# Kernel optimization log

Measured on AMD Instinct MI355X. Metric: run time of the kernel, lower is better.

Reference implementation:

```python
import jax, jax.numpy as jnp
import numpy as np

FEAT_DIM = 4
TOKEN_DIM = 256
HIDDEN = [256, 256]
B, N, T = 512, 512, 4
BN_EPS = 1e-5


def setup_inputs() -> dict:
    key = jax.random.key(0)
    ks = jax.random.split(key, 10)
    bbox_ltwh = jax.random.uniform(ks[0], (B, N, T, FEAT_DIM), dtype=jnp.float32)
    mask = jax.random.randint(ks[1], (B, N), 0, 2).astype(bool)
    # MLP params: Linear(4->256)+BN+ReLU, Linear(256->256)+BN+ReLU, Linear(256->256)
    def lin(k, fan_in, fan_out):
        bound = 1.0 / np.sqrt(fan_in)
        kw, kb = jax.random.split(k)
        W = jax.random.uniform(kw, (fan_in, fan_out), minval=-bound, maxval=bound, dtype=jnp.float32)
        b = jax.random.uniform(kb, (fan_out,), minval=-bound, maxval=bound, dtype=jnp.float32)
        return W, b
    W1, b1 = lin(ks[2], FEAT_DIM, HIDDEN[0])
    W2, b2 = lin(ks[3], HIDDEN[0], HIDDEN[1])
    W3, b3 = lin(ks[4], HIDDEN[1], TOKEN_DIM)
    g1 = jnp.ones((HIDDEN[0],), jnp.float32); be1 = jnp.zeros((HIDDEN[0],), jnp.float32)
    g2 = jnp.ones((HIDDEN[1],), jnp.float32); be2 = jnp.zeros((HIDDEN[1],), jnp.float32)
    return {"bbox_ltwh": bbox_ltwh, "mask": mask,
            "W1": W1, "b1": b1, "g1": g1, "be1": be1,
            "W2": W2, "b2": b2, "g2": g2, "be2": be2,
            "W3": W3, "b3": b3}


def _masked_bn(h, m, cnt, gamma, beta):
    # BatchNorm1d (training mode) over only the valid (masked-in) rows.
    mu = jnp.sum(h * m, axis=0) / cnt
    var = jnp.sum(jnp.square(h - mu) * m, axis=0) / cnt
    return (h - mu) * jax.lax.rsqrt(var + BN_EPS) * gamma + beta


def reference(bbox_ltwh, mask, W1, b1, g1, be1, W2, b2, g2, be2, W3, b3):
    # last bbox of each tracklet: [B, N, 4] -> [B*N, 4]
    x = bbox_ltwh[:, :, 0].reshape(-1, FEAT_DIM)
    m = mask.reshape(-1).astype(x.dtype)[:, None]  # [B*N, 1]
    cnt = jnp.maximum(jnp.sum(m), 1.0)
    # Equivalent to gather(valid) -> MLP -> scatter into zeros: compute on all
    # rows with BN statistics taken over valid rows only, then zero invalid rows.
    h = jax.nn.relu(_masked_bn(x @ W1 + b1, m, cnt, g1, be1))
    h = jax.nn.relu(_masked_bn(h @ W2 + b2, m, cnt, g2, be2))
    h = h @ W3 + b3
    out = (h * m).reshape(B, N, TOKEN_DIM)
    return out
```

## Files before the change

### kernel.cpp

```cpp
#include <hip/hip_runtime.h>

typedef __attribute__((ext_vector_type(8))) short short8;
typedef __attribute__((ext_vector_type(4))) float f32x4;

#define M_ROWS (512*512)
#define NTILES (M_ROWS/64)
#define GRID_SETUP 512
#define GRID_STATS 512
#define GRID_MLP 512
#define ROWS_MLP (M_ROWS/GRID_MLP)
#define TILES_MLP (ROWS_MLP/64)
#define BN_EPS_F 1e-5f

#define WS_P1   64
#define WS_CNT  12352
#define WS_A1   12416
#define WS_D1   13440
#define WS_A2   13696
#define WS_C2   13952
#define WS_W2T  14336
#define WS_W3T  47104
#define WS_P2   79872

__device__ __forceinline__ float load_mask(const void* mp, int fmt, int row) {
  return fmt ? (((const unsigned char*)mp)[row] ? 1.f : 0.f)
             : (((const int*)mp)[row] ? 1.f : 0.f);
}

__device__ __forceinline__ ushort f2bf(float f) {
  unsigned int u = __float_as_uint(f);
  u += 0x7FFFu + ((u >> 16) & 1u);
  return (ushort)(u >> 16);
}

__device__ __forceinline__ void barrier_lds() {
  __builtin_amdgcn_sched_barrier(0);
  asm volatile("s_waitcnt lgkmcnt(0)");
  __builtin_amdgcn_sched_barrier(0);
  __builtin_amdgcn_s_barrier();
  __builtin_amdgcn_sched_barrier(0);
}

__device__ __forceinline__ void compute_h1(
    const float (*xs)[4], ushort* h1s, int t,
    const float a1c[4][2], const float d1c[2]) {
  const int c0 = (t & 127) * 2;
  const int r0 = (t >> 7) * 32;
  #pragma unroll 4
  for (int rr = 0; rr < 32; ++rr) {
    const int r = r0 + rr;
    const f32x4 xv = *(const f32x4*)&xs[r][0];
    float v0 = d1c[0], v1 = d1c[1];
    v0 = fmaf(xv.x, a1c[0][0], v0); v1 = fmaf(xv.x, a1c[0][1], v1);
    v0 = fmaf(xv.y, a1c[1][0], v0); v1 = fmaf(xv.y, a1c[1][1], v1);
    v0 = fmaf(xv.z, a1c[2][0], v0); v1 = fmaf(xv.z, a1c[2][1], v1);
    v0 = fmaf(xv.w, a1c[3][0], v0); v1 = fmaf(xv.w, a1c[3][1], v1);
    v0 = fmaxf(v0, 0.f); v1 = fmaxf(v1, 0.f);
    unsigned int pk = (unsigned int)f2bf(v0) | ((unsigned int)f2bf(v1) << 16);
    unsigned int byte = (unsigned int)r*512u + (unsigned int)c0*2u;
    byte ^= (unsigned int)(r & 7) << 4;
    *(unsigned int*)((char*)h1s + byte) = pk;
  }
}

__device__ __forceinline__ void load_aF(const ushort* h1s, int lane, int ks,
                                        int kb, short8 aF[4]) {
  #pragma unroll
  for (int rf = 0; rf < 4; ++rf) {
    const int row = rf*16 + (lane & 15);
    unsigned int byte = (unsigned int)row*512u + (unsigned int)((ks*32 + kb)*2);
    byte ^= (unsigned int)(row & 7) << 4;
    aF[rf] = *(const short8*)((const char*)h1s + byte);
  }
}

__device__ __forceinline__ void gemm_reg(const ushort* h1s,
    const short8 Br[4][8], int lane, f32x4 acc[4][4]) {
  const int kb = (lane >> 4) * 8;
  #pragma unroll
  for (int ks = 0; ks < 8; ++ks) {
    short8 aF[4];
    load_aF(h1s, lane, ks, kb, aF);
    #pragma unroll
    for (int cf = 0; cf < 4; ++cf)
      #pragma unroll
      for (int rf = 0; rf < 4; ++rf)
        acc[rf][cf] = __builtin_amdgcn_mfma_f32_16x16x32_bf16(
            aF[rf], Br[cf][ks], acc[rf][cf], 0, 0, 0);
  }
}

__device__ __forceinline__ void load_B(const ushort* __restrict__ Wt,
                                       int lane, int wave, short8 Br[4][8]) {
  const int kb = (lane >> 4) * 8;
  const ushort* wp = Wt + (size_t)(wave*64 + (lane & 15))*256 + kb;
  #pragma unroll
  for (int cf = 0; cf < 4; ++cf)
    #pragma unroll
    for (int ks = 0; ks < 8; ++ks)
      Br[cf][ks] = *(const short8*)(wp + cf*4096 + ks*32);
}

__global__ __launch_bounds__(256) void setup_kernel(
    const float* __restrict__ bbox, const void* __restrict__ maskp,
    const float* __restrict__ W2, const float* __restrict__ W3,
    float* __restrict__ wsf) {
  __shared__ int s_fmt;
  __shared__ float red[256][22];
  const int t = threadIdx.x, b = blockIdx.x;
  if (t == 0) s_fmt = 0;
  __syncthreads();
  {
    const uint4 v = ((const uint4*)maskp)[t];
    if (((v.x | v.y | v.z | v.w) & 0xFFFFFF00u) != 0u) s_fmt = 1;
  }
  __syncthreads();
  const int fmt = s_fmt;

  float own[21];
  #pragma unroll
  for (int i = 0; i < 21; ++i) own[i] = 0.f;
  #pragma unroll
  for (int i = 0; i < 2; ++i) {
    const int row = b*512 + i*256 + t;
    const float m = load_mask(maskp, fmt, row);
    if (m != 0.f) {
      float4 x4 = *(const float4*)(bbox + (size_t)row * 16);
      float xv[4] = {x4.x, x4.y, x4.z, x4.w};
      own[0] += 1.f;
      #pragma unroll
      for (int i2 = 0; i2 < 4; ++i2) {
        own[1+i2] += xv[i2];
        #pragma unroll
        for (int j = 0; j < 4; ++j)
          own[5+i2*4+j] = fmaf(xv[i2], xv[j], own[5+i2*4+j]);
      }
    }
  }
  #pragma unroll
  for (int s = 0; s < 21; ++s) red[t][s] = own[s];
  __syncthreads();
  for (int off = 128; off > 0; off >>= 1) {
    if (t < off) {
      #pragma unroll
      for (int s = 0; s < 21; ++s) red[t][s] += red[t+off][s];
    }
    __syncthreads();
  }
  if (t < 21) wsf[WS_P1 + b*24 + t] = red[0][t];

  if (b < 256) {
    ((ushort*)(wsf + WS_W2T))[t*256 + b] = f2bf(W2[b*256 + t]);
  } else {
    const int bb = b - 256;
    ((ushort*)(wsf + WS_W3T))[t*256 + bb] = f2bf(W3[bb*256 + t]);
  }
}

__global__ __launch_bounds__(256) void finalize1_kernel(
    const float* __restrict__ part, const float* __restrict__ W1,
    const float* __restrict__ b1, const float* __restrict__ g1,
    const float* __restrict__ be1, float* __restrict__ wsf) {
  __shared__ float red[256][22];
  __shared__ float sarr[21];
  const int t = threadIdx.x;
  #pragma unroll
  for (int s = 0; s < 21; ++s)
    red[t][s] = part[t*24 + s] + part[(t+256)*24 + s];
  __syncthreads();
  for (int off = 128; off > 0; off >>= 1) {
    if (t < off) {
      #pragma unroll
      for (int s = 0; s < 21; ++s) red[t][s] += red[t+off][s];
    }
    __syncthreads();
  }
  if (t < 21) sarr[t] = red[0][t];
  __syncthreads();
  float s[21];
  #pragma unroll
  for (int i = 0; i < 21; ++i) s[i] = sarr[i];
  const float cnt = fmaxf(s[0], 1.f);
  float w[4] = {W1[t], W1[256+t], W1[512+t], W1[768+t]};
  const float b1f = b1[t];
  float sw = 0.f;
  #pragma unroll
  for (int k = 0; k < 4; ++k) sw = fmaf(s[1+k], w[k], sw);
  float qf = 0.f;
  #pragma unroll
  for (int i = 0; i < 4; ++i)
    #pragma unroll
    for (int j = 0; j < 4; ++j) qf = fmaf(s[5+i*4+j]*w[i], w[j], qf);
  const float mu  = sw/cnt + b1f;
  const float eh2 = (qf + 2.f*b1f*sw)/cnt + b1f*b1f;
  const float var = fmaxf(eh2 - mu*mu, 0.f);
  const float a1  = g1[t] * rsqrtf(var + BN_EPS_F);
  const float c1  = be1[t] - mu*a1;
  #pragma unroll
  for (int k = 0; k < 4; ++k) wsf[WS_A1 + k*256 + t] = w[k]*a1;
  wsf[WS_D1 + t] = fmaf(b1f, a1, c1);
  if (t == 0) wsf[WS_CNT] = cnt;
}

__global__ __launch_bounds__(256, 2) void stats2_mfma(
    const float* __restrict__ bbox, const void* __restrict__ maskp,
    const float* wsf, const float* __restrict__ b2,
    float* __restrict__ part2) {
  __shared__ float xs[64][4];
  __shared__ float ms[64];
  __shared__ ushort h1s[64*256];
  __shared__ int s_fmt;
  const int t = threadIdx.x, lane = t & 63, wave = t >> 6;
  if (t == 0) s_fmt = 0;
  __syncthreads();
  {
    const uint4 v = ((const uint4*)maskp)[t];
    if (((v.x | v.y | v.z | v.w) & 0xFFFFFF00u) != 0u) s_fmt = 1;
  }
  __syncthreads();
  const int fmt = s_fmt;
  float a1c[4][2], d1c[2];
  {
    const int c0 = (t & 127) * 2;
    #pragma unroll
    for (int j = 0; j < 4; ++j) {
      a1c[j][0] = wsf[WS_A1 + j*256 + c0];
      a1c[j][1] = wsf[WS_A1 + j*256 + c0 + 1];
    }
    d1c[0] = wsf[WS_D1 + c0]; d1c[1] = wsf[WS_D1 + c0 + 1];
  }
  short8 B2r[4][8];
  load_B((const ushort*)(wsf + WS_W2T), lane, wave, B2r);
  float b2v[4];
  #pragma unroll
  for (int cf = 0; cf < 4; ++cf) b2v[cf] = b2[wave*64 + cf*16 + (lane & 15)];
  float pS[4] = {0,0,0,0}, pQ[4] = {0,0,0,0};

  for (int tile = blockIdx.x; tile < NTILES; tile += GRID_STATS) {
    const int row0 = tile << 6;
    __syncthreads();
    if (t < 64) {
      float4 x4 = *(const float4*)(bbox + (size_t)(row0 + t) * 16);
      xs[t][0] = x4.x; xs[t][1] = x4.y; xs[t][2] = x4.z; xs[t][3] = x4.w;
      ms[t] = load_mask(maskp, fmt, row0 + t);
    }
    __syncthreads();
    compute_h1(xs, h1s, t, a1c, d1c);
    __syncthreads();
    f32x4 acc[4][4];
    #pragma unroll
    for (int rf = 0; rf < 4; ++rf)
      #pragma unroll
      for (int cf = 0; cf < 4; ++cf)
        acc[rf][cf] = (f32x4){b2v[cf], b2v[cf], b2v[cf], b2v[cf]};
    gemm_reg(h1s, B2r, lane, acc);
    float mr[4][4];
    #pragma unroll
    for (int rf = 0; rf < 4; ++rf)
      #pragma unroll
      for (int r = 0; r < 4; ++r)
        mr[rf][r] = ms[rf*16 + ((lane >> 4) * 4) + r];
    #pragma unroll
    for (int cf = 0; cf < 4; ++cf)
      #pragma unroll
      for (int rf = 0; rf < 4; ++rf)
        #pragma unroll
        for (int r = 0; r < 4; ++r) {
          const float m = mr[rf][r];
          const float v = acc[rf][cf][r];
          pS[cf] = fmaf(m, v, pS[cf]);
          pQ[cf] = fmaf(m*v, v, pQ[cf]);
        }
  }
  #pragma unroll
  for (int cf = 0; cf < 4; ++cf) {
    pS[cf] += __shfl_xor(pS[cf], 16); pS[cf] += __shfl_xor(pS[cf], 32);
    pQ[cf] += __shfl_xor(pQ[cf], 16); pQ[cf] += __shfl_xor(pQ[cf], 32);
  }
  if (lane < 16) {
    #pragma unroll
    for (int cf = 0; cf < 4; ++cf) {
      const int col = wave*64 + cf*16 + lane;
      part2[(size_t)blockIdx.x*512 + col] = pS[cf];
      part2[(size_t)blockIdx.x*512 + 256 + col] = pQ[cf];
    }
  }
}

__global__ __launch_bounds__(256) void finalize2_kernel(
    float* __restrict__ wsf, const float* __restrict__ g2,
    const float* __restrict__ be2) {
  const int f = blockIdx.x, t = threadIdx.x;
  const float* part2 = wsf + WS_P2;
  float s1 = 0.f, s2 = 0.f;
  for (int b = t; b < GRID_STATS; b += 256) {
    s1 += part2[(size_t)b*512 + f];
    s2 += part2[(size_t)b*512 + 256 + f];
  }
  __shared__ float r1[256], r2[256];
  r1[t] = s1; r2[t] = s2;
  __syncthreads();
  for (int off = 128; off > 0; off >>= 1) {
    if (t < off) { r1[t] += r1[t+off]; r2[t] += r2[t+off]; }
    __syncthreads();
  }
  if (t == 0) {
    const float cnt = wsf[WS_CNT];
    const float mu  = r1[0]/cnt;
    const float var = fmaxf(r2[0]/cnt - mu*mu, 0.f);
    const float a2  = g2[f] * rsqrtf(var + BN_EPS_F);
    wsf[WS_A2 + f] = a2;
    wsf[WS_C2 + f] = be2[f] - mu*a2;
  }
}

__global__ __launch_bounds__(256, 1) void mlp3_mfma(
    const float* __restrict__ bbox, const void* __restrict__ maskp,
    const float* wsf, const float* __restrict__ b2,
    const float* __restrict__ b3, float* __restrict__ out) {
  __shared__ ushort h1s[64*256];
  __shared__ float xst[ROWS_MLP][4];
  __shared__ float mst[ROWS_MLP];
  __shared__ int s_fmt;
  const int t = threadIdx.x, lane = t & 63, wave = t >> 6;
  if (t == 0) s_fmt = 0;
  __syncthreads();
  {
    const uint4 v = ((const uint4*)maskp)[t];
    if (((v.x | v.y | v.z | v.w) & 0xFFFFFF00u) != 0u) s_fmt = 1;
  }
  __syncthreads();
  const int fmt = s_fmt;
  const int row_base = blockIdx.x * ROWS_MLP;

  #pragma unroll
  for (int i = 0; i < ROWS_MLP/256; ++i) {
    const int r = i*256 + t;
    float4 x4 = *(const float4*)(bbox + (size_t)(row_base + r) * 16);
    xst[r][0] = x4.x; xst[r][1] = x4.y; xst[r][2] = x4.z; xst[r][3] = x4.w;
    mst[r] = load_mask(maskp, fmt, row_base + r);
  }
  float a1c[4][2], d1c[2];
  {
    const int c0 = (t & 127) * 2;
    #pragma unroll
    for (int j = 0; j < 4; ++j) {
      a1c[j][0] = wsf[WS_A1 + j*256 + c0];
      a1c[j][1] = wsf[WS_A1 + j*256 + c0 + 1];
    }
    d1c[0] = wsf[WS_D1 + c0]; d1c[1] = wsf[WS_D1 + c0 + 1];
  }
  short8 B2r[4][8], B3r[4][8];
  load_B((const ushort*)(wsf + WS_W2T), lane, wave, B2r);
  load_B((const ushort*)(wsf + WS_W3T), lane, wave, B3r);
  float b2v[4], b3v[4], a2v[4], c2v[4];
  #pragma unroll
  for (int cf = 0; cf < 4; ++cf) {
    const int col = wave*64 + cf*16 + (lane & 15);
    b2v[cf] = b2[col]; b3v[cf] = b3[col];
    a2v[cf] = wsf[WS_A2 + col]; c2v[cf] = wsf[WS_C2 + col];
  }
  __syncthreads();

  for (int tile = 0; tile < TILES_MLP; ++tile) {
    const int r0 = tile * 64;
    compute_h1(&xst[r0], h1s, t, a1c, d1c);
    barrier_lds();
    f32x4 acc[4][4];
    #pragma unroll
    for (int rf = 0; rf < 4; ++rf)
      #pragma unroll
      for (int cf = 0; cf < 4; ++cf)
        acc[rf][cf] = (f32x4){b2v[cf], b2v[cf], b2v[cf], b2v[cf]};
    gemm_reg(h1s, B2r, lane, acc);
    barrier_lds();
    #pragma unroll
    for (int rf = 0; rf < 4; ++rf)
      #pragma unroll
      for (int cf = 0; cf < 4; ++cf) {
        const int col = wave*64 + cf*16 + (lane & 15);
        #pragma unroll
        for (int r = 0; r < 4; ++r) {
          const float v = fmaxf(fmaf(acc[rf][cf][r], a2v[cf], c2v[cf]), 0.f);
          const int row = rf*16 + ((lane >> 4) * 4) + r;
          unsigned int byte = (unsigned int)row*512u + (unsigned int)col*2u;
          byte ^= (unsigned int)(row & 7) << 4;
          *(ushort*)((char*)h1s + byte) = f2bf(v);
        }
      }
    barrier_lds();
    #pragma unroll
    for (int rf = 0; rf < 4; ++rf)
      #pragma unroll
      for (int cf = 0; cf < 4; ++cf)
        acc[rf][cf] = (f32x4){b3v[cf], b3v[cf], b3v[cf], b3v[cf]};
    gemm_reg(h1s, B3r, lane, acc);
    float mr[4][4];
    #pragma unroll
    for (int rf = 0; rf < 4; ++rf)
      #pragma unroll
      for (int r = 0; r < 4; ++r)
        mr[rf][r] = mst[r0 + rf*16 + ((lane >> 4) * 4) + r];
    #pragma unroll
    for (int rf = 0; rf < 4; ++rf)
      #pragma unroll
      for (int cf = 0; cf < 4; ++cf) {
        const int col = wave*64 + cf*16 + (lane & 15);
        #pragma unroll
        for (int r = 0; r < 4; ++r) {
          const int lrow = rf*16 + ((lane >> 4) * 4) + r;
          out[(size_t)(row_base + r0 + lrow)*256 + col] =
              acc[rf][cf][r] * mr[rf][r];
        }
      }
    barrier_lds();
  }
}

extern "C" void kernel_launch(void* const* d_in, const int* in_sizes, int n_in,
                              void* d_out, int out_size, void* d_ws, size_t ws_size,
                              hipStream_t stream) {
  (void)in_sizes; (void)n_in; (void)out_size; (void)ws_size;
  const float* bbox = (const float*)d_in[0];
  const void*  maskp= d_in[1];
  const float* W1 = (const float*)d_in[2];
  const float* b1 = (const float*)d_in[3];
  const float* g1 = (const float*)d_in[4];
  const float* be1= (const float*)d_in[5];
  const float* W2 = (const float*)d_in[6];
  const float* b2 = (const float*)d_in[7];
  const float* g2 = (const float*)d_in[8];
  const float* be2= (const float*)d_in[9];
  const float* W3 = (const float*)d_in[10];
  const float* b3 = (const float*)d_in[11];
  float* out = (float*)d_out;
  float* wsf = (float*)d_ws;

  hipLaunchKernelGGL(setup_kernel, dim3(GRID_SETUP), dim3(256), 0, stream,
                     bbox, maskp, W2, W3, wsf);
  hipLaunchKernelGGL(finalize1_kernel, dim3(1), dim3(256), 0, stream,
                     wsf + WS_P1, W1, b1, g1, be1, wsf);
  hipLaunchKernelGGL(stats2_mfma, dim3(GRID_STATS), dim3(256), 0, stream,
                     bbox, maskp, wsf, b2, wsf + WS_P2);
  hipLaunchKernelGGL(finalize2_kernel, dim3(256), dim3(256), 0, stream,
                     wsf, g2, be2);
  hipLaunchKernelGGL(mlp3_mfma, dim3(GRID_MLP), dim3(256), 0, stream,
                     bbox, maskp, wsf, b2, b3, out);
}
```

Before: 214.2 us.

## Stage layer-2 pre-BN activations in bf16 workspace to skip recomputing GEMM2

The stats pass now writes the layer-2 pre-BN outputs as bf16 to a workspace buffer. A new final kernel reads them back, applies BN2 and ReLU while building the MFMA A-fragments, and runs only GEMM3, so layer 1 and GEMM2 are not computed a second time. This trades a 128 MB bf16 write and read for the removed matmul, and it only takes effect when the workspace is large enough. The fallback path also changes its grid size from 512 to 256 blocks.

```diff
diff --git a/kernel.cpp b/kernel.cpp
--- a/kernel.cpp
+++ b/kernel.cpp
@@ -7,9 +7,12 @@
 #define NTILES (M_ROWS/64)
 #define GRID_SETUP 512
 #define GRID_STATS 512
-#define GRID_MLP 512
-#define ROWS_MLP (M_ROWS/GRID_MLP)
-#define TILES_MLP (ROWS_MLP/64)
+#define GRID_MLP3 512
+#define ROWS_MLP3 (M_ROWS/GRID_MLP3)
+#define TILES_MLP3 (ROWS_MLP3/64)
+#define GRID_FB 256
+#define ROWS_FB (M_ROWS/GRID_FB)
+#define TILES_FB (ROWS_FB/64)
 #define BN_EPS_F 1e-5f
 
 #define WS_P1   64
@@ -21,6 +24,8 @@
 #define WS_W2T  14336
 #define WS_W3T  47104
 #define WS_P2   79872
+#define WS_H2   (WS_P2 + 512*512)
+#define WS_NEED ((size_t)WS_H2*4 + (size_t)M_ROWS*256*2)
 
 __device__ __forceinline__ float load_mask(const void* mp, int fmt, int row) {
   return fmt ? (((const unsigned char*)mp)[row] ? 1.f : 0.f)
@@ -205,7 +210,7 @@
 __global__ __launch_bounds__(256, 2) void stats2_mfma(
     const float* __restrict__ bbox, const void* __restrict__ maskp,
     const float* wsf, const float* __restrict__ b2,
-    float* __restrict__ part2) {
+    float* __restrict__ part2, ushort* __restrict__ h2stg) {
   __shared__ float xs[64][4];
   __shared__ float ms[64];
   __shared__ ushort h1s[64*256];
@@ -271,6 +276,32 @@
           pS[cf] = fmaf(m, v, pS[cf]);
           pQ[cf] = fmaf(m*v, v, pQ[cf]);
         }
+    if (h2stg) {
+      __syncthreads();
+      #pragma unroll
+      for (int rf = 0; rf < 4; ++rf)
+        #pragma unroll
+        for (int cf = 0; cf < 4; ++cf) {
+          const int col = wave*64 + cf*16 + (lane & 15);
+          #pragma unroll
+          for (int r = 0; r < 4; ++r) {
+            const int row = rf*16 + ((lane >> 4) * 4) + r;
+            unsigned int byte = (unsigned int)row*512u + (unsigned int)col*2u;
+            byte ^= (unsigned int)(row & 7) << 4;
+            *(ushort*)((char*)h1s + byte) = f2bf(acc[rf][cf][r]);
+          }
+        }
+      __syncthreads();
+      #pragma unroll
+      for (int i = 0; i < 8; ++i) {
+        const int v = i*2048 + t*8;
+        const int row = v >> 8, col = v & 255;
+        unsigned int byte = (unsigned int)row*512u + (unsigned int)col*2u;
+        byte ^= (unsigned int)(row & 7) << 4;
+        short8 d = *(const short8*)((const char*)h1s + byte);
+        *(short8*)(h2stg + (size_t)(row0 + row)*256 + col) = d;
+      }
+    }
   }
   #pragma unroll
   for (int cf = 0; cf < 4; ++cf) {
@@ -314,13 +345,98 @@
   }
 }
 
+__global__ __launch_bounds__(256, 2) void mlp3b(
+    const void* __restrict__ maskp, const float* wsf,
+    const ushort* __restrict__ h2stg, const float* __restrict__ b3,
+    float* __restrict__ out) {
+  __shared__ float a2s[256], c2s[256];
+  __shared__ float mst[ROWS_MLP3];
+  __shared__ int s_fmt;
+  const int t = threadIdx.x, lane = t & 63, wave = t >> 6;
+  if (t == 0) s_fmt = 0;
+  __syncthreads();
+  {
+    const uint4 v = ((const uint4*)maskp)[t];
+    if (((v.x | v.y | v.z | v.w) & 0xFFFFFF00u) != 0u) s_fmt = 1;
+  }
+  __syncthreads();
+  const int fmt = s_fmt;
+  const int row_base = blockIdx.x * ROWS_MLP3;
+  a2s[t] = wsf[WS_A2 + t];
+  c2s[t] = wsf[WS_C2 + t];
+  #pragma unroll
+  for (int i = 0; i < ROWS_MLP3/256; ++i) {
+    const int r = i*256 + t;
+    mst[r] = load_mask(maskp, fmt, row_base + r);
+  }
+  short8 B3r[4][8];
+  load_B((const ushort*)(wsf + WS_W3T), lane, wave, B3r);
+  float b3v[4];
+  #pragma unroll
+  for (int cf = 0; cf < 4; ++cf) b3v[cf] = b3[wave*64 + cf*16 + (lane & 15)];
+  const int kb = (lane >> 4) * 8;
+  __syncthreads();
+
+  for (int tile = 0; tile < TILES_MLP3; ++tile) {
+    const int row0g = row_base + tile*64;
+    f32x4 acc[4][4];
+    #pragma unroll
+    for (int rf = 0; rf < 4; ++rf)
+      #pragma unroll
+      for (int cf = 0; cf < 4; ++cf)
+        acc[rf][cf] = (f32x4){b3v[cf], b3v[cf], b3v[cf], b3v[cf]};
+    #pragma unroll
+    for (int ks = 0; ks < 8; ++ks) {
+      const int k0 = ks*32 + kb;
+      const f32x4 a2lo = *(const f32x4*)&a2s[k0];
+      const f32x4 a2hi = *(const f32x4*)&a2s[k0+4];
+      const f32x4 c2lo = *(const f32x4*)&c2s[k0];
+      const f32x4 c2hi = *(const f32x4*)&c2s[k0+4];
+      short8 aF[4];
+      #pragma unroll
+      for (int rf = 0; rf < 4; ++rf) {
+        const int grow = row0g + rf*16 + (lane & 15);
+        short8 raw = *(const short8*)(h2stg + (size_t)grow*256 + k0);
+        #pragma unroll
+        for (int j = 0; j < 4; ++j) {
+          float f0 = __uint_as_float(((unsigned)(ushort)raw[j]) << 16);
+          float v0 = fmaxf(fmaf(f0, a2lo[j], c2lo[j]), 0.f);
+          aF[rf][j] = (short)f2bf(v0);
+          float f1 = __uint_as_float(((unsigned)(ushort)raw[4+j]) << 16);
+          float v1 = fmaxf(fmaf(f1, a2hi[j], c2hi[j]), 0.f);
+          aF[rf][4+j] = (short)f2bf(v1);
+        }
+      }
+      #pragma unroll
+      for (int cf = 0; cf < 4; ++cf)
+        #pragma unroll
+        for (int rf = 0; rf < 4; ++rf)
+          acc[rf][cf] = __builtin_amdgcn_mfma_f32_16x16x32_bf16(
+              aF[rf], B3r[cf][ks], acc[rf][cf], 0, 0, 0);
+    }
+    const int r0 = tile * 64;
+    #pragma unroll
+    for (int rf = 0; rf < 4; ++rf)
+      #pragma unroll
+      for (int cf = 0; cf < 4; ++cf) {
+        const int col = wave*64 + cf*16 + (lane & 15);
+        #pragma unroll
+        for (int r = 0; r < 4; ++r) {
+          const int lrow = rf*16 + ((lane >> 4) * 4) + r;
+          out[(size_t)(row_base + r0 + lrow)*256 + col] =
+              acc[rf][cf][r] * mst[r0 + lrow];
+        }
+      }
+  }
+}
+
 __global__ __launch_bounds__(256, 1) void mlp3_mfma(
     const float* __restrict__ bbox, const void* __restrict__ maskp,
     const float* wsf, const float* __restrict__ b2,
     const float* __restrict__ b3, float* __restrict__ out) {
   __shared__ ushort h1s[64*256];
-  __shared__ float xst[ROWS_MLP][4];
-  __shared__ float mst[ROWS_MLP];
+  __shared__ float xst[ROWS_FB][4];
+  __shared__ float mst[ROWS_FB];
   __shared__ int s_fmt;
   const int t = threadIdx.x, lane = t & 63, wave = t >> 6;
   if (t == 0) s_fmt = 0;
@@ -331,10 +447,10 @@
   }
   __syncthreads();
   const int fmt = s_fmt;
-  const int row_base = blockIdx.x * ROWS_MLP;
-
-  #pragma unroll
-  for (int i = 0; i < ROWS_MLP/256; ++i) {
+  const int row_base = blockIdx.x * ROWS_FB;
+
+  #pragma unroll
+  for (int i = 0; i < ROWS_FB/256; ++i) {
     const int r = i*256 + t;
     float4 x4 = *(const float4*)(bbox + (size_t)(row_base + r) * 16);
     xst[r][0] = x4.x; xst[r][1] = x4.y; xst[r][2] = x4.z; xst[r][3] = x4.w;
@@ -362,7 +478,7 @@
   }
   __syncthreads();
 
-  for (int tile = 0; tile < TILES_MLP; ++tile) {
+  for (int tile = 0; tile < TILES_FB; ++tile) {
     const int r0 = tile * 64;
     compute_h1(&xst[r0], h1s, t, a1c, d1c);
     barrier_lds();
@@ -420,7 +536,7 @@
 extern "C" void kernel_launch(void* const* d_in, const int* in_sizes, int n_in,
                               void* d_out, int out_size, void* d_ws, size_t ws_size,
                               hipStream_t stream) {
-  (void)in_sizes; (void)n_in; (void)out_size; (void)ws_size;
+  (void)in_sizes; (void)n_in; (void)out_size;
   const float* bbox = (const float*)d_in[0];
   const void*  maskp= d_in[1];
   const float* W1 = (const float*)d_in[2];
@@ -435,15 +551,22 @@
   const float* b3 = (const float*)d_in[11];
   float* out = (float*)d_out;
   float* wsf = (float*)d_ws;
+  const bool split = (ws_size >= WS_NEED);
+  ushort* h2stg = split ? (ushort*)(wsf + WS_H2) : (ushort*)nullptr;
 
   hipLaunchKernelGGL(setup_kernel, dim3(GRID_SETUP), dim3(256), 0, stream,
                      bbox, maskp, W2, W3, wsf);
   hipLaunchKernelGGL(finalize1_kernel, dim3(1), dim3(256), 0, stream,
                      wsf + WS_P1, W1, b1, g1, be1, wsf);
   hipLaunchKernelGGL(stats2_mfma, dim3(GRID_STATS), dim3(256), 0, stream,
-                     bbox, maskp, wsf, b2, wsf + WS_P2);
+                     bbox, maskp, wsf, b2, wsf + WS_P2, h2stg);
   hipLaunchKernelGGL(finalize2_kernel, dim3(256), dim3(256), 0, stream,
                      wsf, g2, be2);
-  hipLaunchKernelGGL(mlp3_mfma, dim3(GRID_MLP), dim3(256), 0, stream,
-                     bbox, maskp, wsf, b2, b3, out);
-}
+  if (split) {
+    hipLaunchKernelGGL(mlp3b, dim3(GRID_MLP3), dim3(256), 0, stream,
+                       maskp, wsf, h2stg, b3, out);
+  } else {
+    hipLaunchKernelGGL(mlp3_mfma, dim3(GRID_FB), dim3(256), 0, stream,
+                       bbox, maskp, wsf, b2, b3, out);
+  }
+}
```

New measurement: 537.2 us. +150.9%, slower.
